# Kernel optimization log

Measured on AMD Instinct MI355X. Metric: run time of the kernel, lower is better.

Reference implementation:

```python
import jax, jax.numpy as jnp
import numpy as np

INV_SQRT2 = 0.7071067811865476  # pywt haar: cA=(x0+x1)/sqrt2, cD=(x0-x1)/sqrt2


def haar_dwt2(x):
    # x: (..., H, W) with even H, W. Matches pywt.dwt2 (cA, (cH, cV, cD))
    # keys: cH='da' (detail along rows), cV='ad', cD='dd'.
    aw = (x[..., ::2] + x[..., 1::2]) * INV_SQRT2   # low-pass along W
    dw = (x[..., ::2] - x[..., 1::2]) * INV_SQRT2   # high-pass along W
    LL = (aw[..., ::2, :] + aw[..., 1::2, :]) * INV_SQRT2
    LH = (aw[..., ::2, :] - aw[..., 1::2, :]) * INV_SQRT2  # cH
    HL = (dw[..., ::2, :] + dw[..., 1::2, :]) * INV_SQRT2  # cV
    HH = (dw[..., ::2, :] - dw[..., 1::2, :]) * INV_SQRT2  # cD
    return LL, LH, HL, HH


def _interleave_h(e, o):
    out_shape = e.shape[:-2] + (2 * e.shape[-2], e.shape[-1])
    return jnp.stack([e, o], axis=-2).reshape(out_shape)


def _interleave_w(e, o):
    out_shape = e.shape[:-1] + (2 * e.shape[-1],)
    return jnp.stack([e, o], axis=-1).reshape(out_shape)


def haar_idwt2(LL, LH, HL, HH):
    # exact inverse of haar_dwt2 (== pywt.idwt2 for haar, even sizes)
    aw = _interleave_h((LL + LH) * INV_SQRT2, (LL - LH) * INV_SQRT2)
    dw = _interleave_h((HL + HH) * INV_SQRT2, (HL - HH) * INV_SQRT2)
    return _interleave_w((aw + dw) * INV_SQRT2, (aw - dw) * INV_SQRT2)


def conv2d(x, w, b, stride, pad):
    y = jax.lax.conv_general_dilated(
        x, w, (stride, stride), [(pad, pad), (pad, pad)],
        dimension_numbers=('NCHW', 'OIHW', 'NCHW'))
    return y + b[None, :, None, None]


def conv_transpose2d(x, w, b, stride, pad):
    # torch ConvTranspose2d weight layout: (in, out, kH, kW)
    k = w.shape[2]
    wt = jnp.flip(jnp.transpose(w, (1, 0, 2, 3)), (2, 3))  # -> (out,in,kH,kW)
    p = k - 1 - pad
    y = jax.lax.conv_general_dilated(
        x, wt, (1, 1), [(p, p), (p, p)], lhs_dilation=(stride, stride),
        dimension_numbers=('NCHW', 'OIHW', 'NCHW'))
    return y + b[None, :, None, None]


def setup_inputs() -> dict:
    key = jax.random.key(0)
    k1, k2, k3 = jax.random.split(key, 3)
    B, C, H, W = 32, 3, 512, 512
    x = jax.random.normal(k1, (B, C, H, W), dtype=jnp.float32)
    # kaiming-style init for the small 9->9 convs
    down_w = jax.random.normal(k2, (9, 9, 3, 3), dtype=jnp.float32) * np.sqrt(2.0 / (9 * 9))
    down_b = jnp.zeros((9,), dtype=jnp.float32)
    up_w = jax.random.normal(k3, (9, 9, 4, 4), dtype=jnp.float32) * np.sqrt(2.0 / (9 * 16))
    up_b = jnp.zeros((9,), dtype=jnp.float32)
    return {"x": x, "down_w": down_w, "down_b": down_b, "up_w": up_w, "up_b": up_b}


def reference(x, down_w, down_b, up_w, up_b):
    B, C, H, W = x.shape
    # ---- encode ----
    LL1, LH1, HL1, HH1 = haar_dwt2(x)      # (B,C,H/2,W/2)
    LL2, LH2, HL2, HH2 = haar_dwt2(LL1)    # (B,C,H/4,W/4)
    level2 = jnp.stack([LL2, LH2, HL2, HH2], axis=2).reshape(B, C * 4, H // 4, W // 4)
    level1 = jnp.stack([LH1, HL1, HH1], axis=2).reshape(B, C * 3, H // 2, W // 2)
    level1_down = conv2d(level1, down_w, down_b, stride=2, pad=1)  # (B,9,H/4,W/4)
    z = jnp.concatenate([level2, level1_down], axis=1)             # (B,21,H/4,W/4)
    # ---- decode ----
    l2 = z[:, :4 * C].reshape(B, C, 4, H // 4, W // 4)
    l1 = conv_transpose2d(z[:, 4 * C:], up_w, up_b, stride=2, pad=1)
    l1 = l1.reshape(B, C, 3, H // 2, W // 2)
    LL1r = haar_idwt2(l2[:, :, 0], l2[:, :, 1], l2[:, :, 2], l2[:, :, 3])
    x_rec = haar_idwt2(LL1r, l1[:, :, 0], l1[:, :, 1], l1[:, :, 2])
    return x_rec
```

## Files before the change

### kernel.cpp

```cpp
#include <hip/hip_runtime.h>


#define BB 32

__global__ __launch_bounds__(256) void k0_rearrange(
    const float* __restrict__ dw, const float* __restrict__ uw,
    float* __restrict__ wd, float* __restrict__ wu, float* __restrict__ zp)
{
    const int t = threadIdx.x;
    for (int i = t; i < 729; i += 256) {
        const int o    = i % 9;
        const int band = (i / 9) % 3;
        const int q    = (i / 27) % 3;
        const int a    = (i / 81) % 3;
        const int ch   = i / 243;
        wd[i] = 0.5f * dw[o * 81 + (ch * 3 + band) * 9 + a * 3 + q];
    }
    for (int i = t; i < 1296; i += 256) {
        const int o = i % 9; int r = i / 9;
        const int dj = r & 1; const int di = (r >> 1) & 1; r >>= 2;
        const int ct = r & 1; const int rt = (r >> 1) & 1; const int cin = r >> 2;
        wu[i] = uw[cin * 144 + o * 16 + (3 - di - 2 * rt) * 4 + (3 - dj - 2 * ct)];
    }
    if (t < 16) zp[t] = 0.f;
}

__device__ __forceinline__ void gload16(const float* gp, float* lp) {
    __builtin_amdgcn_global_load_lds(
        (const __attribute__((address_space(1))) void*)gp,
        (__attribute__((address_space(3))) void*)lp, 16, 0, 0);
}

__global__ __launch_bounds__(256) void k1_dwt_down(
    const float* __restrict__ x,
    const float* __restrict__ wd,
    const float* __restrict__ db,
    const float* __restrict__ zp,
    float* __restrict__ LL1,
    float* __restrict__ y)
{
    __shared__ float xs[3 * 5120];

    const int t    = threadIdx.x;
    const int bid  = blockIdx.x;
    const int swz  = (bid & 7) * 256 + (bid >> 3);
    const int b    = swz >> 6;
    const int tile = swz & 63;
    const int i0   = (tile >> 3) << 4;
    const int j0   = (tile & 7) << 4;
    const int ti   = t >> 4;
    const int tj   = t & 15;
    const int I    = i0 + ti;
    const int J    = j0 + tj;
    const int gr0  = 4 * i0 - 2;
    const int gc0  = 4 * j0 - 4;

#pragma unroll
    for (int ch = 0; ch < 3; ++ch) {
        const float* xc = x + ((size_t)b * 3 + ch) * (512 * 512);
#pragma unroll
        for (int n = 0; n < 5; ++n) {
            const int idx = n * 256 + t;
            const int lr  = idx / 17;
            const int f4c = idx - lr * 17;
            const int gr  = gr0 + lr;
            const bool ok = (idx < 1122) && (gr >= 0) && !(f4c == 0 && j0 == 0);
            const float* gp = ok ? (xc + (size_t)gr * 512 + gc0 + 4 * f4c) : zp;
            gload16(gp, &xs[(ch * 1280 + idx) * 4]);
        }
    }

    float acc[9];
#pragma unroll
    for (int o = 0; o < 9; ++o) acc[o] = db[o];

    __syncthreads();

#pragma unroll
    for (int ch = 0; ch < 3; ++ch) {
        const float* xb  = xs + ch * 5120;
        const float* wch = wd + ch * 243;
        float* llc = LL1 + ((size_t)b * 3 + ch) * (256 * 256);

#pragma unroll
        for (int a = 0; a < 3; ++a) {
            float2 p[2][3];
#pragma unroll
            for (int rr = 0; rr < 2; ++rr)
#pragma unroll
                for (int k = 0; k < 3; ++k)
                    p[rr][k] = *reinterpret_cast<const float2*>(
                        &xb[(4 * ti + 2 * a + rr) * 68 + 4 * tj + 2 + 2 * k]);

            float lh[3], hl[3], hh[3], llv1, llv2;
            {
                const float s0 = p[0][0].x + p[0][0].y, d0 = p[0][0].x - p[0][0].y;
                const float s1 = p[1][0].x + p[1][0].y, d1 = p[1][0].x - p[1][0].y;
                lh[0] = s0 - s1; hl[0] = d0 + d1; hh[0] = d0 - d1;
            }
            {
                const float s0 = p[0][1].x + p[0][1].y, d0 = p[0][1].x - p[0][1].y;
                const float s1 = p[1][1].x + p[1][1].y, d1 = p[1][1].x - p[1][1].y;
                lh[1] = s0 - s1; hl[1] = d0 + d1; hh[1] = d0 - d1;
                llv1 = (s0 + s1) * 0.5f;
            }
            {
                const float s0 = p[0][2].x + p[0][2].y, d0 = p[0][2].x - p[0][2].y;
                const float s1 = p[1][2].x + p[1][2].y, d1 = p[1][2].x - p[1][2].y;
                lh[2] = s0 - s1; hl[2] = d0 + d1; hh[2] = d0 - d1;
                llv2 = (s0 + s1) * 0.5f;
            }

            if (a >= 1) {
                float2 w2; w2.x = llv1; w2.y = llv2;
                *reinterpret_cast<float2*>(llc + (size_t)(2 * I - 1 + a) * 256 + 2 * J) = w2;
            }

            const float* wg = wch + a * 81;
#pragma unroll
            for (int q = 0; q < 3; ++q) {
                const float* w0 = wg + q * 27;
#pragma unroll
                for (int o = 0; o < 9; ++o) acc[o] += lh[q] * w0[o];
#pragma unroll
                for (int o = 0; o < 9; ++o) acc[o] += hl[q] * w0[9 + o];
#pragma unroll
                for (int o = 0; o < 9; ++o) acc[o] += hh[q] * w0[18 + o];
            }
        }
    }

#pragma unroll
    for (int o = 0; o < 9; ++o)
        y[(((size_t)b * 9 + o) * 128 + I) * 128 + J] = acc[o];
}

__global__ __launch_bounds__(256, 4) void k2_up_idwt(
    const float* __restrict__ yg,
    const float* __restrict__ wu,
    const float* __restrict__ ub,
    const float* __restrict__ LL1,
    float* __restrict__ out)
{
    __shared__ float ysh[9][18][19];

    const int t    = threadIdx.x;
    const int b    = blockIdx.x >> 6;
    const int tile = blockIdx.x & 63;
    const int r0   = (tile >> 3) << 5;
    const int c0   = (tile & 7) << 5;
    const int p0   = (r0 >> 1) - 1;
    const int q0   = (c0 >> 1) - 1;

    for (int item = t; item < 9 * 324; item += 256) {
        const int cin = item / 324;
        int rem       = item - cin * 324;
        const int lp  = rem / 18;
        const int lq  = rem - lp * 18;
        const int p   = p0 + lp, q = q0 + lq;
        float v = 0.f;
        if (p >= 0 && p < 128 && q >= 0 && q < 128)
            v = yg[(((size_t)b * 9 + cin) * 128 + p) * 128 + q];
        ysh[cin][lp][lq] = v;
    }
    __syncthreads();

    const int i2 = t >> 4;
    const int j2 = t & 15;

    float acc[2][2][9];
#pragma unroll
    for (int di = 0; di < 2; ++di)
#pragma unroll
        for (int dj = 0; dj < 2; ++dj)
#pragma unroll
            for (int o = 0; o < 9; ++o) acc[di][dj][o] = ub[o];

    for (int cin = 0; cin < 9; ++cin) {
        float yv[3][3];
#pragma unroll
        for (int r = 0; r < 3; ++r)
#pragma unroll
            for (int c = 0; c < 3; ++c)
                yv[r][c] = ysh[cin][i2 + r][j2 + c];
        const float* wc = wu + cin * 144;
#pragma unroll
        for (int rt = 0; rt < 2; ++rt)
#pragma unroll
            for (int ct = 0; ct < 2; ++ct) {
                const float* wg = wc + (rt * 2 + ct) * 36;
#pragma unroll
                for (int di = 0; di < 2; ++di)
#pragma unroll
                    for (int dj = 0; dj < 2; ++dj) {
                        const float vv = yv[di + rt][dj + ct];
                        const float* w9 = wg + (di * 2 + dj) * 9;
#pragma unroll
                        for (int o = 0; o < 9; ++o)
                            acc[di][dj][o] += vv * w9[o];
                    }
            }
    }

#pragma unroll
    for (int cc = 0; cc < 3; ++cc) {
#pragma unroll
        for (int di = 0; di < 2; ++di) {
            const int I = r0 + 2 * i2 + di;
            const int J = c0 + 2 * j2;
            const float2 llv = *reinterpret_cast<const float2*>(
                LL1 + (((size_t)b * 3 + cc) * 256 + I) * 256 + J);
            float4 top, bot;
            {
                const float ll = llv.x;
                const float lh = acc[di][0][cc * 3 + 0];
                const float hl = acc[di][0][cc * 3 + 1];
                const float hh = acc[di][0][cc * 3 + 2];
                const float e0 = ll + lh, od0 = ll - lh;
                const float e1 = hl + hh, od1 = hl - hh;
                top.x = (e0 + e1) * 0.5f; top.y = (e0 - e1) * 0.5f;
                bot.x = (od0 + od1) * 0.5f; bot.y = (od0 - od1) * 0.5f;
            }
            {
                const float ll = llv.y;
                const float lh = acc[di][1][cc * 3 + 0];
                const float hl = acc[di][1][cc * 3 + 1];
                const float hh = acc[di][1][cc * 3 + 2];
                const float e0 = ll + lh, od0 = ll - lh;
                const float e1 = hl + hh, od1 = hl - hh;
                top.z = (e0 + e1) * 0.5f; top.w = (e0 - e1) * 0.5f;
                bot.z = (od0 + od1) * 0.5f; bot.w = (od0 - od1) * 0.5f;
            }
            float* op = out + (((size_t)b * 3 + cc) * 512 + 2 * I) * 512 + 2 * J;
            *reinterpret_cast<float4*>(op) = top;
            *reinterpret_cast<float4*>(op + 512) = bot;
        }
    }
}

extern "C" void kernel_launch(void* const* d_in, const int* in_sizes, int n_in,
                              void* d_out, int out_size, void* d_ws, size_t ws_size,
                              hipStream_t stream) {
    const float* x  = (const float*)d_in[0];
    const float* dw = (const float*)d_in[1];
    const float* db = (const float*)d_in[2];
    const float* uw = (const float*)d_in[3];
    const float* ub = (const float*)d_in[4];
    float* outp = (float*)d_out;

    float* wsf = (float*)d_ws;
    float* wd  = wsf;
    float* wu  = wsf + 768;
    float* zp  = wsf + 2240;
    float* LL1 = wsf + 2304;
    float* y   = LL1 + (size_t)BB * 3 * 256 * 256;

    k0_rearrange<<<dim3(1), dim3(256), 0, stream>>>(dw, uw, wd, wu, zp);
    k1_dwt_down<<<dim3(BB * 64), dim3(256), 0, stream>>>(x, wd, db, zp, LL1, y);
    k2_up_idwt<<<dim3(BB * 64), dim3(256), 0, stream>>>(y, wu, ub, LL1, outp);
}
```

Before: 82.65 us.

## Split k1 channels across three thread groups with LDS partial-sum reduction

The DWT+down-conv kernel now launches 768 threads per block, and each 256-thread group handles one input channel instead of one thread looping over all three. Groups 1 and 2 write their 9 partial conv accumulators to shared memory, and group 0 sums them and writes y. This spreads the per-thread work three ways and adds parallelism. In exchange it costs extra LDS traffic, a second barrier, about 18 KB more shared memory, and a tighter register budget from launch_bounds(768,6).

```diff
diff --git a/kernel.cpp b/kernel.cpp
--- a/kernel.cpp
+++ b/kernel.cpp
@@ -31,7 +31,7 @@
         (__attribute__((address_space(3))) void*)lp, 16, 0, 0);
 }
 
-__global__ __launch_bounds__(256) void k1_dwt_down(
+__global__ __launch_bounds__(768, 6) void k1_dwt_down(
     const float* __restrict__ x,
     const float* __restrict__ wd,
     const float* __restrict__ db,
@@ -40,47 +40,48 @@
     float* __restrict__ y)
 {
     __shared__ float xs[3 * 5120];
+    __shared__ float part[2][256][9];
 
     const int t    = threadIdx.x;
+    const int g    = t >> 8;
+    const int tl   = t & 255;
     const int bid  = blockIdx.x;
     const int swz  = (bid & 7) * 256 + (bid >> 3);
     const int b    = swz >> 6;
     const int tile = swz & 63;
     const int i0   = (tile >> 3) << 4;
     const int j0   = (tile & 7) << 4;
-    const int ti   = t >> 4;
-    const int tj   = t & 15;
+    const int ti   = tl >> 4;
+    const int tj   = tl & 15;
     const int I    = i0 + ti;
     const int J    = j0 + tj;
     const int gr0  = 4 * i0 - 2;
     const int gc0  = 4 * j0 - 4;
 
-#pragma unroll
-    for (int ch = 0; ch < 3; ++ch) {
-        const float* xc = x + ((size_t)b * 3 + ch) * (512 * 512);
+    {
+        const float* xc = x + ((size_t)b * 3 + g) * (512 * 512);
 #pragma unroll
         for (int n = 0; n < 5; ++n) {
-            const int idx = n * 256 + t;
+            const int idx = n * 256 + tl;
             const int lr  = idx / 17;
             const int f4c = idx - lr * 17;
             const int gr  = gr0 + lr;
             const bool ok = (idx < 1122) && (gr >= 0) && !(f4c == 0 && j0 == 0);
             const float* gp = ok ? (xc + (size_t)gr * 512 + gc0 + 4 * f4c) : zp;
-            gload16(gp, &xs[(ch * 1280 + idx) * 4]);
+            gload16(gp, &xs[(g * 1280 + idx) * 4]);
         }
     }
 
     float acc[9];
 #pragma unroll
-    for (int o = 0; o < 9; ++o) acc[o] = db[o];
+    for (int o = 0; o < 9; ++o) acc[o] = (g == 0) ? db[o] : 0.f;
 
     __syncthreads();
 
-#pragma unroll
-    for (int ch = 0; ch < 3; ++ch) {
-        const float* xb  = xs + ch * 5120;
-        const float* wch = wd + ch * 243;
-        float* llc = LL1 + ((size_t)b * 3 + ch) * (256 * 256);
+    {
+        const float* xb  = xs + g * 5120;
+        const float* wch = wd + g * 243;
+        float* llc = LL1 + ((size_t)b * 3 + g) * (256 * 256);
 
 #pragma unroll
         for (int a = 0; a < 3; ++a) {
@@ -130,9 +131,18 @@
         }
     }
 
-#pragma unroll
-    for (int o = 0; o < 9; ++o)
-        y[(((size_t)b * 9 + o) * 128 + I) * 128 + J] = acc[o];
+    if (g > 0) {
+#pragma unroll
+        for (int o = 0; o < 9; ++o) part[g - 1][tl][o] = acc[o];
+    }
+    __syncthreads();
+    if (g == 0) {
+#pragma unroll
+        for (int o = 0; o < 9; ++o) {
+            const float v = acc[o] + part[0][tl][o] + part[1][tl][o];
+            y[(((size_t)b * 9 + o) * 128 + I) * 128 + J] = v;
+        }
+    }
 }
 
 __global__ __launch_bounds__(256, 4) void k2_up_idwt(
@@ -256,6 +266,6 @@
     float* y   = LL1 + (size_t)BB * 3 * 256 * 256;
 
     k0_rearrange<<<dim3(1), dim3(256), 0, stream>>>(dw, uw, wd, wu, zp);
-    k1_dwt_down<<<dim3(BB * 64), dim3(256), 0, stream>>>(x, wd, db, zp, LL1, y);
+    k1_dwt_down<<<dim3(BB * 64), dim3(768), 0, stream>>>(x, wd, db, zp, LL1, y);
     k2_up_idwt<<<dim3(BB * 64), dim3(256), 0, stream>>>(y, wu, ub, LL1, outp);
 }
```

After: 128.9 us. 1.56x slower.

## Split k1 output channels across two thread halves with smaller tiles

Applied to the files above, without the earlier changes.

Halves the k1 spatial tile to 8x16 outputs and splits the nine output channels between two 128-thread groups (5 and 4). This cuts LDS per block and accumulator registers and doubles the block count, aiming for higher occupancy. The cost is that both groups recompute the same Haar transforms and the halo rows are loaded proportionally more often. The grid grows to 4096 blocks with launch bounds 256,4.

```diff
diff --git a/kernel.cpp b/kernel.cpp
--- a/kernel.cpp
+++ b/kernel.cpp
@@ -31,7 +31,7 @@
         (__attribute__((address_space(3))) void*)lp, 16, 0, 0);
 }
 
-__global__ __launch_bounds__(256) void k1_dwt_down(
+__global__ __launch_bounds__(256, 4) void k1_dwt_down(
     const float* __restrict__ x,
     const float* __restrict__ wd,
     const float* __restrict__ db,
@@ -39,46 +39,55 @@
     float* __restrict__ LL1,
     float* __restrict__ y)
 {
-    __shared__ float xs[3 * 5120];
+    __shared__ float xs[3 * 3072];
 
     const int t    = threadIdx.x;
     const int bid  = blockIdx.x;
-    const int swz  = (bid & 7) * 256 + (bid >> 3);
-    const int b    = swz >> 6;
-    const int tile = swz & 63;
-    const int i0   = (tile >> 3) << 4;
-    const int j0   = (tile & 7) << 4;
-    const int ti   = t >> 4;
-    const int tj   = t & 15;
-    const int I    = i0 + ti;
-    const int J    = j0 + tj;
-    const int gr0  = 4 * i0 - 2;
-    const int gc0  = 4 * j0 - 4;
+    const int swz  = (bid & 7) * 512 + (bid >> 3);
+    const int b    = swz >> 7;
+    const int tin  = swz & 127;
+    const int I0   = (tin >> 3) * 8;
+    const int J0   = (tin & 7) * 16;
+    const int gr0  = 4 * I0 - 2;
+    const int gc0  = 4 * J0 - 4;
 
 #pragma unroll
     for (int ch = 0; ch < 3; ++ch) {
         const float* xc = x + ((size_t)b * 3 + ch) * (512 * 512);
 #pragma unroll
-        for (int n = 0; n < 5; ++n) {
+        for (int n = 0; n < 3; ++n) {
             const int idx = n * 256 + t;
             const int lr  = idx / 17;
             const int f4c = idx - lr * 17;
             const int gr  = gr0 + lr;
-            const bool ok = (idx < 1122) && (gr >= 0) && !(f4c == 0 && j0 == 0);
+            const bool ok = (idx < 578) && (gr >= 0) && !(f4c == 0 && J0 == 0);
             const float* gp = ok ? (xc + (size_t)gr * 512 + gc0 + 4 * f4c) : zp;
-            gload16(gp, &xs[(ch * 1280 + idx) * 4]);
+            gload16(gp, &xs[(ch * 768 + idx) * 4]);
         }
     }
 
-    float acc[9];
-#pragma unroll
-    for (int o = 0; o < 9; ++o) acc[o] = db[o];
+    const int og = t >> 7;
+    const int tl = t & 127;
+    const int ti = tl >> 4;
+    const int tj = tl & 15;
+    const int I  = I0 + ti;
+    const int J  = J0 + tj;
+
+    float acc[5];
+    if (og == 0) {
+#pragma unroll
+        for (int o = 0; o < 5; ++o) acc[o] = db[o];
+    } else {
+#pragma unroll
+        for (int o = 0; o < 4; ++o) acc[o] = db[5 + o];
+        acc[4] = 0.f;
+    }
 
     __syncthreads();
 
 #pragma unroll
     for (int ch = 0; ch < 3; ++ch) {
-        const float* xb  = xs + ch * 5120;
+        const float* xb  = xs + ch * 3072;
         const float* wch = wd + ch * 243;
         float* llc = LL1 + ((size_t)b * 3 + ch) * (256 * 256);
 
@@ -111,7 +120,7 @@
                 llv2 = (s0 + s1) * 0.5f;
             }
 
-            if (a >= 1) {
+            if (og == 0 && a >= 1) {
                 float2 w2; w2.x = llv1; w2.y = llv2;
                 *reinterpret_cast<float2*>(llc + (size_t)(2 * I - 1 + a) * 256 + 2 * J) = w2;
             }
@@ -120,19 +129,35 @@
 #pragma unroll
             for (int q = 0; q < 3; ++q) {
                 const float* w0 = wg + q * 27;
-#pragma unroll
-                for (int o = 0; o < 9; ++o) acc[o] += lh[q] * w0[o];
-#pragma unroll
-                for (int o = 0; o < 9; ++o) acc[o] += hl[q] * w0[9 + o];
-#pragma unroll
-                for (int o = 0; o < 9; ++o) acc[o] += hh[q] * w0[18 + o];
+                const float vlh = lh[q], vhl = hl[q], vhh = hh[q];
+                if (og == 0) {
+#pragma unroll
+                    for (int o = 0; o < 5; ++o) acc[o] += vlh * w0[o];
+#pragma unroll
+                    for (int o = 0; o < 5; ++o) acc[o] += vhl * w0[9 + o];
+#pragma unroll
+                    for (int o = 0; o < 5; ++o) acc[o] += vhh * w0[18 + o];
+                } else {
+#pragma unroll
+                    for (int o = 0; o < 4; ++o) acc[o] += vlh * w0[5 + o];
+#pragma unroll
+                    for (int o = 0; o < 4; ++o) acc[o] += vhl * w0[14 + o];
+#pragma unroll
+                    for (int o = 0; o < 4; ++o) acc[o] += vhh * w0[23 + o];
+                }
             }
         }
     }
 
-#pragma unroll
-    for (int o = 0; o < 9; ++o)
-        y[(((size_t)b * 9 + o) * 128 + I) * 128 + J] = acc[o];
+    if (og == 0) {
+#pragma unroll
+        for (int o = 0; o < 5; ++o)
+            y[(((size_t)b * 9 + o) * 128 + I) * 128 + J] = acc[o];
+    } else {
+#pragma unroll
+        for (int o = 0; o < 4; ++o)
+            y[(((size_t)b * 9 + 5 + o) * 128 + I) * 128 + J] = acc[o];
+    }
 }
 
 __global__ __launch_bounds__(256, 4) void k2_up_idwt(
@@ -256,6 +281,6 @@
     float* y   = LL1 + (size_t)BB * 3 * 256 * 256;
 
     k0_rearrange<<<dim3(1), dim3(256), 0, stream>>>(dw, uw, wd, wu, zp);
-    k1_dwt_down<<<dim3(BB * 64), dim3(256), 0, stream>>>(x, wd, db, zp, LL1, y);
+    k1_dwt_down<<<dim3(4096), dim3(256), 0, stream>>>(x, wd, db, zp, LL1, y);
     k2_up_idwt<<<dim3(BB * 64), dim3(256), 0, stream>>>(y, wu, ub, LL1, outp);
 }
```

After: 87.85 us. 6.3% more time.

## Fuse DWT+down-conv and up-conv+IDWT into one kernel with halo recompute

Applied to the files above, without the earlier changes.

Merges the two main kernels into a single kernel per 32x32 output tile. It computes the wavelet bands, the LL1 tile and the down-conv output (with halo) in shared memory, then runs the transposed conv and inverse DWT directly. The global round-trip of LL1 and the intermediate y is removed. In exchange, halo regions of the down-conv are recomputed, shared memory use per block is higher, and the down-conv work is split unevenly across two thread halves.

```diff
diff --git a/kernel.cpp b/kernel.cpp
--- a/kernel.cpp
+++ b/kernel.cpp
@@ -31,209 +31,148 @@
         (__attribute__((address_space(3))) void*)lp, 16, 0, 0);
 }
 
-__global__ __launch_bounds__(256) void k1_dwt_down(
+#define TAP(CH, A)                                                             \
+    {                                                                          \
+        const float* wg = wd + ((CH) * 3 + (A)) * 81;                          \
+        _Pragma("unroll")                                                      \
+        for (int q3 = 0; q3 < 3; ++q3) {                                       \
+            const float* w0 = wg + q3 * 27;                                    \
+            const float vlh = bnd[(((CH) * 3 + 0) * 21 + 2 * lp + (A)) * 21 + 2 * lq + q3]; \
+            const float vhl = bnd[(((CH) * 3 + 1) * 21 + 2 * lp + (A)) * 21 + 2 * lq + q3]; \
+            const float vhh = bnd[(((CH) * 3 + 2) * 21 + 2 * lp + (A)) * 21 + 2 * lq + q3]; \
+            _Pragma("unroll") for (int o = 0; o < 9; ++o) acc[o] += vlh * w0[o];       \
+            _Pragma("unroll") for (int o = 0; o < 9; ++o) acc[o] += vhl * w0[9 + o];   \
+            _Pragma("unroll") for (int o = 0; o < 9; ++o) acc[o] += vhh * w0[18 + o];  \
+        }                                                                      \
+    }
+
+__global__ __launch_bounds__(256) void kf_fused(
     const float* __restrict__ x,
     const float* __restrict__ wd,
     const float* __restrict__ db,
+    const float* __restrict__ wu,
+    const float* __restrict__ ub,
     const float* __restrict__ zp,
-    float* __restrict__ LL1,
-    float* __restrict__ y)
+    float* __restrict__ out)
 {
-    __shared__ float xs[3 * 5120];
+    __shared__ float xs[6144];
+    __shared__ float bnd[3969];
+    __shared__ float llt[1323];
+    __shared__ float ysp[1980];
 
     const int t    = threadIdx.x;
     const int bid  = blockIdx.x;
-    const int swz  = (bid & 7) * 256 + (bid >> 3);
-    const int b    = swz >> 6;
-    const int tile = swz & 63;
-    const int i0   = (tile >> 3) << 4;
-    const int j0   = (tile & 7) << 4;
-    const int ti   = t >> 4;
-    const int tj   = t & 15;
-    const int I    = i0 + ti;
-    const int J    = j0 + tj;
-    const int gr0  = 4 * i0 - 2;
-    const int gc0  = 4 * j0 - 4;
+    const int swz  = (bid & 7) * 1024 + (bid >> 3);
+    const int b    = swz >> 8;
+    const int tile = swz & 255;
+    const int tr   = tile >> 4, tc = tile & 15;
+    const int X0r  = 32 * tr - 6;
+    const int X0c  = 32 * tc - 8;
 
 #pragma unroll
     for (int ch = 0; ch < 3; ++ch) {
         const float* xc = x + ((size_t)b * 3 + ch) * (512 * 512);
 #pragma unroll
-        for (int n = 0; n < 5; ++n) {
+        for (int n = 0; n < 2; ++n) {
             const int idx = n * 256 + t;
-            const int lr  = idx / 17;
-            const int f4c = idx - lr * 17;
-            const int gr  = gr0 + lr;
-            const bool ok = (idx < 1122) && (gr >= 0) && !(f4c == 0 && j0 == 0);
-            const float* gp = ok ? (xc + (size_t)gr * 512 + gc0 + 4 * f4c) : zp;
-            gload16(gp, &xs[(ch * 1280 + idx) * 4]);
+            const int lrx = idx / 11;
+            const int f4  = idx - lrx * 11;
+            const int gr  = X0r + lrx;
+            const int gc  = X0c + 4 * f4;
+            const bool ok = (idx < 462) && (gr >= 0) && (gr < 512) &&
+                            (gc >= 0) && (gc < 512);
+            const float* gp = ok ? (xc + (size_t)gr * 512 + gc) : zp;
+            gload16(gp, &xs[(ch * 512 + idx) * 4]);
         }
     }
-
-    float acc[9];
-#pragma unroll
-    for (int o = 0; o < 9; ++o) acc[o] = db[o];
-
     __syncthreads();
 
 #pragma unroll
-    for (int ch = 0; ch < 3; ++ch) {
-        const float* xb  = xs + ch * 5120;
-        const float* wch = wd + ch * 243;
-        float* llc = LL1 + ((size_t)b * 3 + ch) * (256 * 256);
-
-#pragma unroll
-        for (int a = 0; a < 3; ++a) {
-            float2 p[2][3];
-#pragma unroll
-            for (int rr = 0; rr < 2; ++rr)
-#pragma unroll
-                for (int k = 0; k < 3; ++k)
-                    p[rr][k] = *reinterpret_cast<const float2*>(
-                        &xb[(4 * ti + 2 * a + rr) * 68 + 4 * tj + 2 + 2 * k]);
-
-            float lh[3], hl[3], hh[3], llv1, llv2;
-            {
-                const float s0 = p[0][0].x + p[0][0].y, d0 = p[0][0].x - p[0][0].y;
-                const float s1 = p[1][0].x + p[1][0].y, d1 = p[1][0].x - p[1][0].y;
-                lh[0] = s0 - s1; hl[0] = d0 + d1; hh[0] = d0 - d1;
-            }
-            {
-                const float s0 = p[0][1].x + p[0][1].y, d0 = p[0][1].x - p[0][1].y;
-                const float s1 = p[1][1].x + p[1][1].y, d1 = p[1][1].x - p[1][1].y;
-                lh[1] = s0 - s1; hl[1] = d0 + d1; hh[1] = d0 - d1;
-                llv1 = (s0 + s1) * 0.5f;
-            }
-            {
-                const float s0 = p[0][2].x + p[0][2].y, d0 = p[0][2].x - p[0][2].y;
-                const float s1 = p[1][2].x + p[1][2].y, d1 = p[1][2].x - p[1][2].y;
-                lh[2] = s0 - s1; hl[2] = d0 + d1; hh[2] = d0 - d1;
-                llv2 = (s0 + s1) * 0.5f;
-            }
-
-            if (a >= 1) {
-                float2 w2; w2.x = llv1; w2.y = llv2;
-                *reinterpret_cast<float2*>(llc + (size_t)(2 * I - 1 + a) * 256 + 2 * J) = w2;
-            }
-
-            const float* wg = wch + a * 81;
-#pragma unroll
-            for (int q = 0; q < 3; ++q) {
-                const float* w0 = wg + q * 27;
-#pragma unroll
-                for (int o = 0; o < 9; ++o) acc[o] += lh[q] * w0[o];
-#pragma unroll
-                for (int o = 0; o < 9; ++o) acc[o] += hl[q] * w0[9 + o];
-#pragma unroll
-                for (int o = 0; o < 9; ++o) acc[o] += hh[q] * w0[18 + o];
-            }
+    for (int n = 0; n < 6; ++n) {
+        const int it = n * 256 + t;
+        if (it < 1323) {
+            const int ch = it / 441;
+            const int rc = it - ch * 441;
+            const int lr = rc / 21;
+            const int lc = rc - lr * 21;
+            const int base = ch * 2048 + (2 * lr) * 44 + 2 * lc + 2;
+            const float a0 = xs[base],      a1 = xs[base + 1];
+            const float b0 = xs[base + 44], b1 = xs[base + 45];
+            const float s0 = a0 + a1, d0 = a0 - a1;
+            const float s1 = b0 + b1, d1 = b0 - b1;
+            bnd[((ch * 3 + 0) * 21 + lr) * 21 + lc] = s0 - s1;
+            bnd[((ch * 3 + 1) * 21 + lr) * 21 + lc] = d0 + d1;
+            bnd[((ch * 3 + 2) * 21 + lr) * 21 + lc] = d0 - d1;
+            llt[(ch * 21 + lr) * 21 + lc] = (s0 + s1) * 0.5f;
         }
-    }
-
-#pragma unroll
-    for (int o = 0; o < 9; ++o)
-        y[(((size_t)b * 9 + o) * 128 + I) * 128 + J] = acc[o];
-}
-
-__global__ __launch_bounds__(256, 4) void k2_up_idwt(
-    const float* __restrict__ yg,
-    const float* __restrict__ wu,
-    const float* __restrict__ ub,
-    const float* __restrict__ LL1,
-    float* __restrict__ out)
-{
-    __shared__ float ysh[9][18][19];
-
-    const int t    = threadIdx.x;
-    const int b    = blockIdx.x >> 6;
-    const int tile = blockIdx.x & 63;
-    const int r0   = (tile >> 3) << 5;
-    const int c0   = (tile & 7) << 5;
-    const int p0   = (r0 >> 1) - 1;
-    const int q0   = (c0 >> 1) - 1;
-
-    for (int item = t; item < 9 * 324; item += 256) {
-        const int cin = item / 324;
-        int rem       = item - cin * 324;
-        const int lp  = rem / 18;
-        const int lq  = rem - lp * 18;
-        const int p   = p0 + lp, q = q0 + lq;
-        float v = 0.f;
-        if (p >= 0 && p < 128 && q >= 0 && q < 128)
-            v = yg[(((size_t)b * 9 + cin) * 128 + p) * 128 + q];
-        ysh[cin][lp][lq] = v;
     }
     __syncthreads();
 
-    const int i2 = t >> 4;
-    const int j2 = t & 15;
+    {
+        const int h  = t >> 7;
+        const int tl = t & 127;
+        if (tl < 100) {
+            const int lp = tl / 10, lq = tl - lp * 10;
+            const int p  = 8 * tr - 1 + lp;
+            const int q  = 8 * tc - 1 + lq;
+            const bool valid = (p >= 0) && (p < 128) && (q >= 0) && (q < 128);
+            float acc[9];
+#pragma unroll
+            for (int o = 0; o < 9; ++o)
+                acc[o] = (h == 0 && valid) ? db[o] : 0.f;
+            if (valid) {
+                if (h == 0) { TAP(0, 0) TAP(0, 1) TAP(0, 2) TAP(2, 0) }
+                else        { TAP(1, 0) TAP(1, 1) TAP(1, 2) TAP(2, 1) TAP(2, 2) }
+            }
+#pragma unroll
+            for (int o = 0; o < 9; ++o)
+                ysp[((h * 9 + o) * 10 + lp) * 11 + lq] = acc[o];
+        }
+    }
+    __syncthreads();
 
-    float acc[2][2][9];
+    {
+        const int wv = t >> 6, l = t & 63;
+        const int di = wv >> 1, dj = wv & 1;
+        const int qi = l >> 3,  qj = l & 7;
+        float acc9[9];
 #pragma unroll
-    for (int di = 0; di < 2; ++di)
-#pragma unroll
-        for (int dj = 0; dj < 2; ++dj)
-#pragma unroll
-            for (int o = 0; o < 9; ++o) acc[di][dj][o] = ub[o];
-
-    for (int cin = 0; cin < 9; ++cin) {
-        float yv[3][3];
-#pragma unroll
-        for (int r = 0; r < 3; ++r)
-#pragma unroll
-            for (int c = 0; c < 3; ++c)
-                yv[r][c] = ysh[cin][i2 + r][j2 + c];
-        const float* wc = wu + cin * 144;
-#pragma unroll
-        for (int rt = 0; rt < 2; ++rt)
-#pragma unroll
-            for (int ct = 0; ct < 2; ++ct) {
-                const float* wg = wc + (rt * 2 + ct) * 36;
-#pragma unroll
-                for (int di = 0; di < 2; ++di)
-#pragma unroll
-                    for (int dj = 0; dj < 2; ++dj) {
-                        const float vv = yv[di + rt][dj + ct];
-                        const float* w9 = wg + (di * 2 + dj) * 9;
-#pragma unroll
-                        for (int o = 0; o < 9; ++o)
-                            acc[di][dj][o] += vv * w9[o];
-                    }
-            }
-    }
+        for (int o = 0; o < 9; ++o) acc9[o] = ub[o];
 
 #pragma unroll
-    for (int cc = 0; cc < 3; ++cc) {
+        for (int cin = 0; cin < 9; ++cin) {
 #pragma unroll
-        for (int di = 0; di < 2; ++di) {
-            const int I = r0 + 2 * i2 + di;
-            const int J = c0 + 2 * j2;
-            const float2 llv = *reinterpret_cast<const float2*>(
-                LL1 + (((size_t)b * 3 + cc) * 256 + I) * 256 + J);
-            float4 top, bot;
-            {
-                const float ll = llv.x;
-                const float lh = acc[di][0][cc * 3 + 0];
-                const float hl = acc[di][0][cc * 3 + 1];
-                const float hh = acc[di][0][cc * 3 + 2];
-                const float e0 = ll + lh, od0 = ll - lh;
-                const float e1 = hl + hh, od1 = hl - hh;
-                top.x = (e0 + e1) * 0.5f; top.y = (e0 - e1) * 0.5f;
-                bot.x = (od0 + od1) * 0.5f; bot.y = (od0 - od1) * 0.5f;
-            }
-            {
-                const float ll = llv.y;
-                const float lh = acc[di][1][cc * 3 + 0];
-                const float hl = acc[di][1][cc * 3 + 1];
-                const float hh = acc[di][1][cc * 3 + 2];
-                const float e0 = ll + lh, od0 = ll - lh;
-                const float e1 = hl + hh, od1 = hl - hh;
-                top.z = (e0 + e1) * 0.5f; top.w = (e0 - e1) * 0.5f;
-                bot.z = (od0 + od1) * 0.5f; bot.w = (od0 - od1) * 0.5f;
-            }
-            float* op = out + (((size_t)b * 3 + cc) * 512 + 2 * I) * 512 + 2 * J;
-            *reinterpret_cast<float4*>(op) = top;
-            *reinterpret_cast<float4*>(op + 512) = bot;
+            for (int rt = 0; rt < 2; ++rt)
+#pragma unroll
+                for (int ct = 0; ct < 2; ++ct) {
+                    const int row = qi + di + rt;
+                    const int col = qj + dj + ct;
+                    const float vv = ysp[(cin * 10 + row) * 11 + col] +
+                                     ysp[((9 + cin) * 10 + row) * 11 + col];
+                    const float* w9 =
+                        wu + ((cin * 4 + rt * 2 + ct) * 4 + di * 2 + dj) * 9;
+#pragma unroll
+                    for (int o = 0; o < 9; ++o) acc9[o] += vv * w9[o];
+                }
+        }
+
+        const int i = 16 * tr + 2 * qi + di;
+        const int j = 16 * tc + 2 * qj + dj;
+#pragma unroll
+        for (int cc = 0; cc < 3; ++cc) {
+            const float ll = llt[(cc * 21 + 2 * qi + di + 3) * 21 +
+                                 (2 * qj + dj + 3)];
+            const float lh = acc9[cc * 3 + 0];
+            const float hl = acc9[cc * 3 + 1];
+            const float hh = acc9[cc * 3 + 2];
+            const float e0 = ll + lh, od0 = ll - lh;
+            const float e1 = hl + hh, od1 = hl - hh;
+            float2 r0w, r1w;
+            r0w.x = (e0 + e1) * 0.5f;  r0w.y = (e0 - e1) * 0.5f;
+            r1w.x = (od0 + od1) * 0.5f; r1w.y = (od0 - od1) * 0.5f;
+            float* op = out + (((size_t)b * 3 + cc) * 512 + 2 * i) * 512 + 2 * j;
+            *reinterpret_cast<float2*>(op)       = r0w;
+            *reinterpret_cast<float2*>(op + 512) = r1w;
         }
     }
 }
@@ -252,10 +191,7 @@
     float* wd  = wsf;
     float* wu  = wsf + 768;
     float* zp  = wsf + 2240;
-    float* LL1 = wsf + 2304;
-    float* y   = LL1 + (size_t)BB * 3 * 256 * 256;
 
     k0_rearrange<<<dim3(1), dim3(256), 0, stream>>>(dw, uw, wd, wu, zp);
-    k1_dwt_down<<<dim3(BB * 64), dim3(256), 0, stream>>>(x, wd, db, zp, LL1, y);
-    k2_up_idwt<<<dim3(BB * 64), dim3(256), 0, stream>>>(y, wu, ub, LL1, outp);
+    kf_fused<<<dim3(8192), dim3(256), 0, stream>>>(x, wd, db, wu, ub, zp, outp);
 }
```

Result: slower. 144.5 us (+74.8%).
